# Optimization experiments

Measured on AMD Instinct MI355X. Metric: run time of the kernel, lower is better.

Reference implementation:

```python
import jax, jax.numpy as jnp
import numpy as np

TEMPERATURE = 0.6


def setup_inputs() -> dict:
    key = jax.random.key(0)
    k1, k2, k3 = jax.random.split(key, 3)
    B, IN, OUT, C = 8192, 256, 32, 50
    x = jax.random.uniform(k1, (B, IN), dtype=jnp.float32)
    weight = jax.random.normal(k2, (C, OUT, IN), dtype=jnp.float32) * 0.05
    bias = jax.random.normal(k3, (C, 1, OUT), dtype=jnp.float32) * 0.05
    return {"x": x, "weight": weight, "bias": bias}


def reference(x, weight, bias):
    # gamma[c,i] = L1 norm of weight over out dim: sum_o |W[c,o,i]|
    gamma = jnp.sum(jnp.abs(weight), axis=1)            # [C, IN]
    alpha = jax.nn.softmax(gamma / TEMPERATURE, axis=1)  # [C, IN]
    alpha_norm = alpha / jnp.max(alpha, axis=1, keepdims=True)  # [C, IN]
    # gated input per class: [C, B, IN]
    xg = x[None, :, :] * alpha_norm[:, None, :]
    # per-class GEMM: y[c,b,o] = sum_i xg[c,b,i] * W[c,o,i]
    y = jnp.einsum('cbi,coi->cbo', xg, weight) + bias    # [C, B, OUT]
    return jnp.transpose(y, (1, 0, 2))                   # [B, C, OUT]
```

## Files before the change

### kernel.cpp

```cpp
#include <hip/hip_runtime.h>
#include <hip/hip_bf16.h>

typedef __bf16 bf16x8 __attribute__((ext_vector_type(8)));
typedef float  f32x4  __attribute__((ext_vector_type(4)));

#define B_ROWS 8192
#define IN_DIM 256
#define OUT_DIM 32
#define NCLS 50
#define INV_T (1.0f / 0.6f)

#define CVT_BLOCKS 1024
#define PG_BLOCKS 400
#define ROWTILES 16
#define NCHUNK 8

__device__ __forceinline__ void gload_lds16(const void* g, void* l) {
    __builtin_amdgcn_global_load_lds(
        (const __attribute__((address_space(1))) void*)g,
        (__attribute__((address_space(3))) void*)l, 16, 0, 0);
}

__global__ __launch_bounds__(256) void k1_cvt_partial(const float* __restrict__ x,
                                                      const float* __restrict__ w,
                                                      __bf16* __restrict__ xb,
                                                      float* __restrict__ partial) {
    int bid = blockIdx.x;
    if (bid < CVT_BLOCKS) {
        int i = (bid * 256 + threadIdx.x) * 8;
        float4 v0 = *reinterpret_cast<const float4*>(x + i);
        float4 v1 = *reinterpret_cast<const float4*>(x + i + 4);
        bf16x8 r;
        r[0] = (__bf16)v0.x; r[1] = (__bf16)v0.y; r[2] = (__bf16)v0.z; r[3] = (__bf16)v0.w;
        r[4] = (__bf16)v1.x; r[5] = (__bf16)v1.y; r[6] = (__bf16)v1.z; r[7] = (__bf16)v1.w;
        *reinterpret_cast<bf16x8*>(xb + i) = r;
    } else {
        int p = bid - CVT_BLOCKS;
        int c = p >> 3, q = p & 7;
        int i = threadIdx.x;
        const float* wp = w + ((size_t)(c * OUT_DIM + q * 4)) * IN_DIM + i;
        float g = fabsf(wp[0]) + fabsf(wp[IN_DIM]) + fabsf(wp[2 * IN_DIM]) + fabsf(wp[3 * IN_DIM]);
        partial[(size_t)p * IN_DIM + i] = g;
    }
}

__global__ __launch_bounds__(256) void k2_alpha_scale(const float* __restrict__ partial,
                                                      const float* __restrict__ w,
                                                      __bf16* __restrict__ wb) {
    int blk = blockIdx.x;
    int c = blk >> 2;
    int o0 = (blk & 3) * 8;
    int i = threadIdx.x;
    float g = 0.f;
#pragma unroll
    for (int q = 0; q < 8; ++q)
        g += partial[(size_t)(c * 8 + q) * IN_DIM + i];
    float m = g;
#pragma unroll
    for (int s = 1; s < 64; s <<= 1) m = fmaxf(m, __shfl_xor(m, s));
    __shared__ float wm[4];
    if ((threadIdx.x & 63) == 0) wm[threadIdx.x >> 6] = m;
    __syncthreads();
    m = fmaxf(fmaxf(wm[0], wm[1]), fmaxf(wm[2], wm[3]));
    float an = __expf((g - m) * INV_T);
    const float* wr = w + ((size_t)c * OUT_DIM + o0) * IN_DIM + i;
    __bf16* wo = wb + ((size_t)c * OUT_DIM + o0) * IN_DIM + i;
#pragma unroll
    for (int o = 0; o < 8; ++o)
        wo[o * IN_DIM] = (__bf16)(wr[o * IN_DIM] * an);
}

__global__ __launch_bounds__(256, 2) void gemm(const __bf16* __restrict__ xb,
                                               const __bf16* __restrict__ wb,
                                               const float* __restrict__ bias,
                                               float* __restrict__ out) {
    __shared__ __align__(16) char lds[4 * 2 * 8192];

    int bid = blockIdx.x;
    int cp = bid >> 4;
    int rt = bid & (ROWTILES - 1);
    int c0 = cp * 2;
    int row0 = rt * 512;
    int lane = threadIdx.x & 63;
    int w4 = threadIdx.x >> 6;
    int l15 = lane & 15;
    int g = lane >> 4;
    int s31 = lane & 31;
    int lr = lane >> 5;

    char* Abuf0 = lds + w4 * 16384;
    char* Abuf1 = Abuf0 + 8192;

    const char* arows = (const char*)(xb + (size_t)(row0 + w4 * 128) * IN_DIM);
#define STAGE_A(BUF, CHUNK)                                                       \
    _Pragma("unroll") for (int il = 0; il < 8; ++il) {                            \
        int r = (CHUNK) * 16 + 2 * il + lr;                                       \
        gload_lds16(arows + (size_t)r * 512 + ((s31 ^ (r & 15)) * 16),            \
                    (BUF) + il * 1024);                                           \
    }
    STAGE_A(Abuf0, 0)

    const char* wsrc = (const char*)(wb + (size_t)c0 * OUT_DIM * IN_DIM);
#pragma unroll
    for (int j = 0; j < 8; ++j) {
        int re = j * 8 + w4 * 2;
        int r = re + lr;
        gload_lds16(wsrc + (size_t)r * 512 + ((s31 ^ (r & 15)) * 16),
                    lds + (re >> 4) * 16384 + 8192 + (re & 15) * 512);
    }

    asm volatile("s_waitcnt vmcnt(0)" ::: "memory");
    __syncthreads();
    __builtin_amdgcn_sched_barrier(0);

    bf16x8 W[2][16];
#pragma unroll
    for (int ci = 0; ci < 2; ++ci)
#pragma unroll
        for (int kk = 0; kk < 8; ++kk) {
            int slot = (4 * kk + g) ^ l15;
            W[ci][kk]     = *reinterpret_cast<const bf16x8*>(
                lds + (2 * ci) * 16384 + 8192 + l15 * 512 + slot * 16);
            W[ci][8 + kk] = *reinterpret_cast<const bf16x8*>(
                lds + (2 * ci + 1) * 16384 + 8192 + l15 * 512 + slot * 16);
        }
#pragma unroll
    for (int ci = 0; ci < 2; ++ci)
#pragma unroll
        for (int kk = 0; kk < 16; ++kk)
            asm volatile("" : "+v"(W[ci][kk]));
    __builtin_amdgcn_sched_barrier(0);
    __syncthreads();

    float4 bv00 = *reinterpret_cast<const float4*>(bias + c0 * OUT_DIM + g * 4);
    float4 bv01 = *reinterpret_cast<const float4*>(bias + c0 * OUT_DIM + 16 + g * 4);
    float4 bv10 = *reinterpret_cast<const float4*>(bias + (c0 + 1) * OUT_DIM + g * 4);
    float4 bv11 = *reinterpret_cast<const float4*>(bias + (c0 + 1) * OUT_DIM + 16 + g * 4);

    float* orow = out + (size_t)(row0 + w4 * 128 + l15) * (NCLS * OUT_DIM) + c0 * OUT_DIM + g * 4;

#pragma unroll
    for (int k = 0; k < NCHUNK; ++k) {
        char* cur = (k & 1) ? Abuf1 : Abuf0;
        char* nxt = (k & 1) ? Abuf0 : Abuf1;
        if (k + 1 < NCHUNK) {
            STAGE_A(nxt, k + 1)
            asm volatile("s_waitcnt vmcnt(12)" ::: "memory");
        } else {
            asm volatile("s_waitcnt vmcnt(4)" ::: "memory");
        }
        __builtin_amdgcn_sched_barrier(0);

        f32x4 acc00 = {bv00.x, bv00.y, bv00.z, bv00.w};
        f32x4 acc01 = {bv01.x, bv01.y, bv01.z, bv01.w};
        f32x4 acc10 = {bv10.x, bv10.y, bv10.z, bv10.w};
        f32x4 acc11 = {bv11.x, bv11.y, bv11.z, bv11.w};
#pragma unroll
        for (int kk = 0; kk < 8; ++kk) {
            int slot = (4 * kk + g) ^ l15;
            bf16x8 a = *reinterpret_cast<const bf16x8*>(cur + (size_t)l15 * 512 + slot * 16);
            acc00 = __builtin_amdgcn_mfma_f32_16x16x32_bf16(W[0][kk],     a, acc00, 0, 0, 0);
            acc01 = __builtin_amdgcn_mfma_f32_16x16x32_bf16(W[0][8 + kk], a, acc01, 0, 0, 0);
            acc10 = __builtin_amdgcn_mfma_f32_16x16x32_bf16(W[1][kk],     a, acc10, 0, 0, 0);
            acc11 = __builtin_amdgcn_mfma_f32_16x16x32_bf16(W[1][8 + kk], a, acc11, 0, 0, 0);
        }
        float* op = orow + (size_t)k * 16 * (NCLS * OUT_DIM);
        *reinterpret_cast<f32x4*>(op) = acc00;
        *reinterpret_cast<f32x4*>(op + 16) = acc01;
        *reinterpret_cast<f32x4*>(op + OUT_DIM) = acc10;
        *reinterpret_cast<f32x4*>(op + OUT_DIM + 16) = acc11;
    }
#undef STAGE_A
}

extern "C" void kernel_launch(void* const* d_in, const int* in_sizes, int n_in,
                              void* d_out, int out_size, void* d_ws, size_t ws_size,
                              hipStream_t stream) {
    const float* x    = (const float*)d_in[0];
    const float* w    = (const float*)d_in[1];
    const float* bias = (const float*)d_in[2];
    float* out = (float*)d_out;

    __bf16* xb      = (__bf16*)d_ws;
    __bf16* wb      = xb + (size_t)B_ROWS * IN_DIM;
    float*  partial = (float*)(wb + (size_t)NCLS * OUT_DIM * IN_DIM);

    k1_cvt_partial<<<CVT_BLOCKS + PG_BLOCKS, 256, 0, stream>>>(x, w, xb, partial);
    k2_alpha_scale<<<200, 256, 0, stream>>>(partial, w, wb);
    gemm<<<25 * ROWTILES, 256, 0, stream>>>(xb, wb, bias, out);
}
```

Baseline: 30.66 us.

## Fuse weight prep into one kernel and rebalance GEMM grid to 512 blocks

```diff
diff --git a/kernel.cpp b/kernel.cpp
--- a/kernel.cpp
+++ b/kernel.cpp
@@ -11,9 +11,7 @@
 #define INV_T (1.0f / 0.6f)
 
 #define CVT_BLOCKS 1024
-#define PG_BLOCKS 400
-#define ROWTILES 16
-#define NCHUNK 8
+#define GBLOCKS 512
 
 __device__ __forceinline__ void gload_lds16(const void* g, void* l) {
     __builtin_amdgcn_global_load_lds(
@@ -21,10 +19,11 @@
         (__attribute__((address_space(3))) void*)l, 16, 0, 0);
 }
 
-__global__ __launch_bounds__(256) void k1_cvt_partial(const float* __restrict__ x,
-                                                      const float* __restrict__ w,
-                                                      __bf16* __restrict__ xb,
-                                                      float* __restrict__ partial) {
+__global__ __launch_bounds__(256) void prep(const float* __restrict__ x,
+                                            const float* __restrict__ w,
+                                            __bf16* __restrict__ xb,
+                                            __bf16* __restrict__ wb) {
+    __shared__ float wm[4];
     int bid = blockIdx.x;
     if (bid < CVT_BLOCKS) {
         int i = (bid * 256 + threadIdx.x) * 8;
@@ -35,39 +34,24 @@
         r[4] = (__bf16)v1.x; r[5] = (__bf16)v1.y; r[6] = (__bf16)v1.z; r[7] = (__bf16)v1.w;
         *reinterpret_cast<bf16x8*>(xb + i) = r;
     } else {
-        int p = bid - CVT_BLOCKS;
-        int c = p >> 3, q = p & 7;
+        int c = bid - CVT_BLOCKS;
         int i = threadIdx.x;
-        const float* wp = w + ((size_t)(c * OUT_DIM + q * 4)) * IN_DIM + i;
-        float g = fabsf(wp[0]) + fabsf(wp[IN_DIM]) + fabsf(wp[2 * IN_DIM]) + fabsf(wp[3 * IN_DIM]);
-        partial[(size_t)p * IN_DIM + i] = g;
+        const float* wc = w + (size_t)c * OUT_DIM * IN_DIM;
+        float g = 0.f;
+#pragma unroll
+        for (int o = 0; o < OUT_DIM; ++o) g += fabsf(wc[o * IN_DIM + i]);
+        float m = g;
+#pragma unroll
+        for (int s = 1; s < 64; s <<= 1) m = fmaxf(m, __shfl_xor(m, s));
+        if ((threadIdx.x & 63) == 0) wm[threadIdx.x >> 6] = m;
+        __syncthreads();
+        m = fmaxf(fmaxf(wm[0], wm[1]), fmaxf(wm[2], wm[3]));
+        float an = __expf((g - m) * INV_T);
+        __bf16* wbc = wb + (size_t)c * OUT_DIM * IN_DIM;
+#pragma unroll
+        for (int o = 0; o < OUT_DIM; ++o)
+            wbc[o * IN_DIM + i] = (__bf16)(wc[o * IN_DIM + i] * an);
     }
-}
-
-__global__ __launch_bounds__(256) void k2_alpha_scale(const float* __restrict__ partial,
-                                                      const float* __restrict__ w,
-                                                      __bf16* __restrict__ wb) {
-    int blk = blockIdx.x;
-    int c = blk >> 2;
-    int o0 = (blk & 3) * 8;
-    int i = threadIdx.x;
-    float g = 0.f;
-#pragma unroll
-    for (int q = 0; q < 8; ++q)
-        g += partial[(size_t)(c * 8 + q) * IN_DIM + i];
-    float m = g;
-#pragma unroll
-    for (int s = 1; s < 64; s <<= 1) m = fmaxf(m, __shfl_xor(m, s));
-    __shared__ float wm[4];
-    if ((threadIdx.x & 63) == 0) wm[threadIdx.x >> 6] = m;
-    __syncthreads();
-    m = fmaxf(fmaxf(wm[0], wm[1]), fmaxf(wm[2], wm[3]));
-    float an = __expf((g - m) * INV_T);
-    const float* wr = w + ((size_t)c * OUT_DIM + o0) * IN_DIM + i;
-    __bf16* wo = wb + ((size_t)c * OUT_DIM + o0) * IN_DIM + i;
-#pragma unroll
-    for (int o = 0; o < 8; ++o)
-        wo[o * IN_DIM] = (__bf16)(wr[o * IN_DIM] * an);
 }
 
 __global__ __launch_bounds__(256, 2) void gemm(const __bf16* __restrict__ xb,
@@ -77,10 +61,16 @@
     __shared__ __align__(16) char lds[4 * 2 * 8192];
 
     int bid = blockIdx.x;
-    int cp = bid >> 4;
-    int rt = bid & (ROWTILES - 1);
-    int c0 = cp * 2;
-    int row0 = rt * 512;
+    int p = (bid * 25) >> 9;
+    int first = (p * GBLOCKS + 24) / 25;
+    int next  = ((p + 1) * GBLOCKS + 24) / 25;
+    int j = bid - first;
+    int np = next - first;
+    int u0 = (j * 128) / np;
+    int u1 = ((j + 1) * 128) / np;
+    int nch = u1 - u0;
+
+    int c0 = p * 2;
     int lane = threadIdx.x & 63;
     int w4 = threadIdx.x >> 6;
     int l15 = lane & 15;
@@ -91,19 +81,19 @@
     char* Abuf0 = lds + w4 * 16384;
     char* Abuf1 = Abuf0 + 8192;
 
-    const char* arows = (const char*)(xb + (size_t)(row0 + w4 * 128) * IN_DIM);
-#define STAGE_A(BUF, CHUNK)                                                       \
+    const char* arows = (const char*)(xb + (size_t)(u0 * 64 + w4 * 16) * IN_DIM);
+#define STAGE_A(BUF, AP)                                                          \
     _Pragma("unroll") for (int il = 0; il < 8; ++il) {                            \
-        int r = (CHUNK) * 16 + 2 * il + lr;                                       \
-        gload_lds16(arows + (size_t)r * 512 + ((s31 ^ (r & 15)) * 16),            \
+        int r = 2 * il + lr;                                                      \
+        gload_lds16((AP) + (size_t)r * 512 + ((s31 ^ r) * 16),                    \
                     (BUF) + il * 1024);                                           \
     }
-    STAGE_A(Abuf0, 0)
+    STAGE_A(Abuf0, arows)
 
     const char* wsrc = (const char*)(wb + (size_t)c0 * OUT_DIM * IN_DIM);
 #pragma unroll
-    for (int j = 0; j < 8; ++j) {
-        int re = j * 8 + w4 * 2;
+    for (int jw = 0; jw < 8; ++jw) {
+        int re = jw * 8 + w4 * 2;
         int r = re + lr;
         gload_lds16(wsrc + (size_t)r * 512 + ((s31 ^ (r & 15)) * 16),
                     lds + (re >> 4) * 16384 + 8192 + (re & 15) * 512);
@@ -137,14 +127,15 @@
     float4 bv10 = *reinterpret_cast<const float4*>(bias + (c0 + 1) * OUT_DIM + g * 4);
     float4 bv11 = *reinterpret_cast<const float4*>(bias + (c0 + 1) * OUT_DIM + 16 + g * 4);
 
-    float* orow = out + (size_t)(row0 + w4 * 128 + l15) * (NCLS * OUT_DIM) + c0 * OUT_DIM + g * 4;
+    float* orow = out + (size_t)(u0 * 64 + w4 * 16 + l15) * (NCLS * OUT_DIM) + c0 * OUT_DIM + g * 4;
 
-#pragma unroll
-    for (int k = 0; k < NCHUNK; ++k) {
-        char* cur = (k & 1) ? Abuf1 : Abuf0;
-        char* nxt = (k & 1) ? Abuf0 : Abuf1;
-        if (k + 1 < NCHUNK) {
-            STAGE_A(nxt, k + 1)
+    char* cur = Abuf0;
+    char* nxt = Abuf1;
+    const char* anext = arows + 64 * 512;
+
+    for (int k = 0; k < nch; ++k) {
+        if (k + 1 < nch) {
+            STAGE_A(nxt, anext)
             asm volatile("s_waitcnt vmcnt(12)" ::: "memory");
         } else {
             asm volatile("s_waitcnt vmcnt(4)" ::: "memory");
@@ -164,11 +155,14 @@
             acc10 = __builtin_amdgcn_mfma_f32_16x16x32_bf16(W[1][kk],     a, acc10, 0, 0, 0);
             acc11 = __builtin_amdgcn_mfma_f32_16x16x32_bf16(W[1][8 + kk], a, acc11, 0, 0, 0);
         }
-        float* op = orow + (size_t)k * 16 * (NCLS * OUT_DIM);
-        *reinterpret_cast<f32x4*>(op) = acc00;
-        *reinterpret_cast<f32x4*>(op + 16) = acc01;
-        *reinterpret_cast<f32x4*>(op + OUT_DIM) = acc10;
-        *reinterpret_cast<f32x4*>(op + OUT_DIM + 16) = acc11;
+        *reinterpret_cast<f32x4*>(orow) = acc00;
+        *reinterpret_cast<f32x4*>(orow + 16) = acc01;
+        *reinterpret_cast<f32x4*>(orow + OUT_DIM) = acc10;
+        *reinterpret_cast<f32x4*>(orow + OUT_DIM + 16) = acc11;
+
+        char* t = cur; cur = nxt; nxt = t;
+        anext += 64 * 512;
+        orow += (size_t)64 * (NCLS * OUT_DIM);
     }
 #undef STAGE_A
 }
@@ -181,11 +175,9 @@
     const float* bias = (const float*)d_in[2];
     float* out = (float*)d_out;
 
-    __bf16* xb      = (__bf16*)d_ws;
-    __bf16* wb      = xb + (size_t)B_ROWS * IN_DIM;
-    float*  partial = (float*)(wb + (size_t)NCLS * OUT_DIM * IN_DIM);
+    __bf16* xb = (__bf16*)d_ws;
+    __bf16* wb = xb + (size_t)B_ROWS * IN_DIM;
 
-    k1_cvt_partial<<<CVT_BLOCKS + PG_BLOCKS, 256, 0, stream>>>(x, w, xb, partial);
-    k2_alpha_scale<<<200, 256, 0, stream>>>(partial, w, wb);
-    gemm<<<25 * ROWTILES, 256, 0, stream>>>(xb, wb, bias, out);
+    prep<<<CVT_BLOCKS + NCLS, 256, 0, stream>>>(x, w, xb, wb);
+    gemm<<<GBLOCKS, 256, 0, stream>>>(xb, wb, bias, out);
 }
```

Result: slower. 32.83 us (+7.1%).

## Fuse weight gamma/softmax scaling and x conversion into one prep kernel

Applied to the files above, without the earlier changes.

```diff
diff --git a/kernel.cpp b/kernel.cpp
--- a/kernel.cpp
+++ b/kernel.cpp
@@ -11,7 +11,6 @@
 #define INV_T (1.0f / 0.6f)
 
 #define CVT_BLOCKS 1024
-#define PG_BLOCKS 400
 #define ROWTILES 16
 #define NCHUNK 8
 
@@ -21,53 +20,42 @@
         (__attribute__((address_space(3))) void*)l, 16, 0, 0);
 }
 
-__global__ __launch_bounds__(256) void k1_cvt_partial(const float* __restrict__ x,
-                                                      const float* __restrict__ w,
-                                                      __bf16* __restrict__ xb,
-                                                      float* __restrict__ partial) {
+__global__ __launch_bounds__(256) void prep(const float* __restrict__ x,
+                                            const float* __restrict__ w,
+                                            __bf16* __restrict__ xb,
+                                            __bf16* __restrict__ wb) {
+    __shared__ float wm[4];
     int bid = blockIdx.x;
-    if (bid < CVT_BLOCKS) {
-        int i = (bid * 256 + threadIdx.x) * 8;
+    if (bid < NCLS) {
+        int c = bid;
+        int i = threadIdx.x;
+        const float* wc = w + (size_t)c * OUT_DIM * IN_DIM + i;
+        float wv[OUT_DIM];
+#pragma unroll
+        for (int o = 0; o < OUT_DIM; ++o) wv[o] = wc[o * IN_DIM];
+        float gsum = 0.f;
+#pragma unroll
+        for (int o = 0; o < OUT_DIM; ++o) gsum += fabsf(wv[o]);
+        float m = gsum;
+#pragma unroll
+        for (int s = 1; s < 64; s <<= 1) m = fmaxf(m, __shfl_xor(m, s));
+        if ((threadIdx.x & 63) == 0) wm[threadIdx.x >> 6] = m;
+        __syncthreads();
+        m = fmaxf(fmaxf(wm[0], wm[1]), fmaxf(wm[2], wm[3]));
+        float an = __expf((gsum - m) * INV_T);
+        __bf16* wo = wb + (size_t)c * OUT_DIM * IN_DIM + i;
+#pragma unroll
+        for (int o = 0; o < OUT_DIM; ++o)
+            wo[o * IN_DIM] = (__bf16)(wv[o] * an);
+    } else {
+        int i = ((bid - NCLS) * 256 + threadIdx.x) * 8;
         float4 v0 = *reinterpret_cast<const float4*>(x + i);
         float4 v1 = *reinterpret_cast<const float4*>(x + i + 4);
         bf16x8 r;
         r[0] = (__bf16)v0.x; r[1] = (__bf16)v0.y; r[2] = (__bf16)v0.z; r[3] = (__bf16)v0.w;
         r[4] = (__bf16)v1.x; r[5] = (__bf16)v1.y; r[6] = (__bf16)v1.z; r[7] = (__bf16)v1.w;
         *reinterpret_cast<bf16x8*>(xb + i) = r;
-    } else {
-        int p = bid - CVT_BLOCKS;
-        int c = p >> 3, q = p & 7;
-        int i = threadIdx.x;
-        const float* wp = w + ((size_t)(c * OUT_DIM + q * 4)) * IN_DIM + i;
-        float g = fabsf(wp[0]) + fabsf(wp[IN_DIM]) + fabsf(wp[2 * IN_DIM]) + fabsf(wp[3 * IN_DIM]);
-        partial[(size_t)p * IN_DIM + i] = g;
     }
-}
-
-__global__ __launch_bounds__(256) void k2_alpha_scale(const float* __restrict__ partial,
-                                                      const float* __restrict__ w,
-                                                      __bf16* __restrict__ wb) {
-    int blk = blockIdx.x;
-    int c = blk >> 2;
-    int o0 = (blk & 3) * 8;
-    int i = threadIdx.x;
-    float g = 0.f;
-#pragma unroll
-    for (int q = 0; q < 8; ++q)
-        g += partial[(size_t)(c * 8 + q) * IN_DIM + i];
-    float m = g;
-#pragma unroll
-    for (int s = 1; s < 64; s <<= 1) m = fmaxf(m, __shfl_xor(m, s));
-    __shared__ float wm[4];
-    if ((threadIdx.x & 63) == 0) wm[threadIdx.x >> 6] = m;
-    __syncthreads();
-    m = fmaxf(fmaxf(wm[0], wm[1]), fmaxf(wm[2], wm[3]));
-    float an = __expf((g - m) * INV_T);
-    const float* wr = w + ((size_t)c * OUT_DIM + o0) * IN_DIM + i;
-    __bf16* wo = wb + ((size_t)c * OUT_DIM + o0) * IN_DIM + i;
-#pragma unroll
-    for (int o = 0; o < 8; ++o)
-        wo[o * IN_DIM] = (__bf16)(wr[o * IN_DIM] * an);
 }
 
 __global__ __launch_bounds__(256, 2) void gemm(const __bf16* __restrict__ xb,
@@ -102,8 +90,8 @@
 
     const char* wsrc = (const char*)(wb + (size_t)c0 * OUT_DIM * IN_DIM);
 #pragma unroll
-    for (int j = 0; j < 8; ++j) {
-        int re = j * 8 + w4 * 2;
+    for (int jw = 0; jw < 8; ++jw) {
+        int re = jw * 8 + w4 * 2;
         int r = re + lr;
         gload_lds16(wsrc + (size_t)r * 512 + ((s31 ^ (r & 15)) * 16),
                     lds + (re >> 4) * 16384 + 8192 + (re & 15) * 512);
@@ -132,10 +120,10 @@
     __builtin_amdgcn_sched_barrier(0);
     __syncthreads();
 
-    float4 bv00 = *reinterpret_cast<const float4*>(bias + c0 * OUT_DIM + g * 4);
-    float4 bv01 = *reinterpret_cast<const float4*>(bias + c0 * OUT_DIM + 16 + g * 4);
-    float4 bv10 = *reinterpret_cast<const float4*>(bias + (c0 + 1) * OUT_DIM + g * 4);
-    float4 bv11 = *reinterpret_cast<const float4*>(bias + (c0 + 1) * OUT_DIM + 16 + g * 4);
+    f32x4 bv00 = *reinterpret_cast<const f32x4*>(bias + c0 * OUT_DIM + g * 4);
+    f32x4 bv01 = *reinterpret_cast<const f32x4*>(bias + c0 * OUT_DIM + 16 + g * 4);
+    f32x4 bv10 = *reinterpret_cast<const f32x4*>(bias + (c0 + 1) * OUT_DIM + g * 4);
+    f32x4 bv11 = *reinterpret_cast<const f32x4*>(bias + (c0 + 1) * OUT_DIM + 16 + g * 4);
 
     float* orow = out + (size_t)(row0 + w4 * 128 + l15) * (NCLS * OUT_DIM) + c0 * OUT_DIM + g * 4;
 
@@ -151,10 +139,10 @@
         }
         __builtin_amdgcn_sched_barrier(0);
 
-        f32x4 acc00 = {bv00.x, bv00.y, bv00.z, bv00.w};
-        f32x4 acc01 = {bv01.x, bv01.y, bv01.z, bv01.w};
-        f32x4 acc10 = {bv10.x, bv10.y, bv10.z, bv10.w};
-        f32x4 acc11 = {bv11.x, bv11.y, bv11.z, bv11.w};
+        f32x4 acc00 = bv00;
+        f32x4 acc01 = bv01;
+        f32x4 acc10 = bv10;
+        f32x4 acc11 = bv11;
 #pragma unroll
         for (int kk = 0; kk < 8; ++kk) {
             int slot = (4 * kk + g) ^ l15;
@@ -181,11 +169,9 @@
     const float* bias = (const float*)d_in[2];
     float* out = (float*)d_out;
 
-    __bf16* xb      = (__bf16*)d_ws;
-    __bf16* wb      = xb + (size_t)B_ROWS * IN_DIM;
-    float*  partial = (float*)(wb + (size_t)NCLS * OUT_DIM * IN_DIM);
+    __bf16* xb = (__bf16*)d_ws;
+    __bf16* wb = xb + (size_t)B_ROWS * IN_DIM;
 
-    k1_cvt_partial<<<CVT_BLOCKS + PG_BLOCKS, 256, 0, stream>>>(x, w, xb, partial);
-    k2_alpha_scale<<<200, 256, 0, stream>>>(partial, w, wb);
+    prep<<<NCLS + CVT_BLOCKS, 256, 0, stream>>>(x, w, xb, wb);
     gemm<<<25 * ROWTILES, 256, 0, stream>>>(xb, wb, bias, out);
 }
```

Measured after the change: 28.25 us (median of 2 runs). -7.9%, faster.
